# Kernel optimization log

Hardware: AMD Instinct MI355X
Metric: run time of the kernel (lower is better)

The kernel has to match this reference:

```python
import jax, jax.numpy as jnp
import numpy as np

B, S, D = 8, 2048, 256


def setup_inputs() -> dict:
    key = jax.random.key(0)
    k1, k2, k3, k4, k5 = jax.random.split(key, 5)
    head = jax.random.normal(k1, (B, S, D), dtype=jnp.float32)
    dep = jax.random.normal(k2, (B, S, D), dtype=jnp.float32)
    edge_U = jax.random.normal(k3, (D, D), dtype=jnp.float32) / np.sqrt(D)
    edge_W = jax.random.normal(k4, (1, 2 * D), dtype=jnp.float32) / np.sqrt(2 * D)
    edge_b = jax.random.normal(k5, (1,), dtype=jnp.float32)
    return {"head": head, "dep": dep, "edge_U": edge_U, "edge_W": edge_W, "edge_b": edge_b}


def reference(head, dep, edge_U, edge_W, edge_b):
    # t1[b,i,o] = head[b,i,:] @ U @ dep[b,o,:]  -> [B,S,S]
    t1 = jnp.einsum('bid,de,boe->bio', head, edge_U, dep)
    # t2: linear over pairwise concat(head_i, dep_o); decomposes into two
    # broadcast-added matvecs (same math as W @ concat, no [B,S^2,2D] tensor).
    d = head.shape[-1]
    wh, wd = edge_W[0, :d], edge_W[0, d:]
    hs = head @ wh  # [B,S]
    ds = dep @ wd   # [B,S]
    t2 = hs[:, :, None] + ds[:, None, :]  # [B,S,S]
    return t1 + t2 + edge_b[0]
```

## Files before the change

kernel.cpp:

```cpp
#include <hip/hip_runtime.h>
#include <hip/hip_bf16.h>
#include <stdint.h>
#include <stddef.h>

#define B_ 8
#define S_ 2048
#define D_ 256
#define NROWS (B_ * S_)

typedef __attribute__((ext_vector_type(8))) short short8;
typedef __attribute__((ext_vector_type(4))) short short4v;
typedef __attribute__((ext_vector_type(4))) float f32x4;

__device__ __forceinline__ short bf16of(float f) {
  union { float f; unsigned u; } x; x.f = f;
  unsigned r = x.u + 0x7FFFu + ((x.u >> 16) & 1u);
  return (short)(r >> 16);
}

__global__ void k_prep_u(const float* __restrict__ U, short* __restrict__ UT) {
  int n = blockIdx.x;
  int k = threadIdx.x;
  UT[n * D_ + k] = bf16of(U[k * D_ + n]);
}

__global__ void k_rows(const float* __restrict__ head, const float* __restrict__ dep,
                       const float* __restrict__ W,
                       float* __restrict__ hs, float* __restrict__ ds,
                       short* __restrict__ headB, short* __restrict__ depB) {
  const float* X; const float* wv; float* sv; short* XB;
  if (blockIdx.y == 0) { X = head; wv = W;      sv = hs; XB = headB; }
  else                 { X = dep;  wv = W + D_; sv = ds; XB = depB;  }
  const int row = blockIdx.x * 4 + (threadIdx.x >> 6);
  const int l = threadIdx.x & 63;
  const float4 v  = *(const float4*)(X + (size_t)row * D_ + l * 4);
  const float4 wq = *(const float4*)(wv + l * 4);
  short4v pk;
  pk[0] = bf16of(v.x); pk[1] = bf16of(v.y); pk[2] = bf16of(v.z); pk[3] = bf16of(v.w);
  *(short4v*)(XB + (size_t)row * D_ + l * 4) = pk;
  float p = v.x * wq.x + v.y * wq.y + v.z * wq.z + v.w * wq.w;
  p += __shfl_xor(p, 1); p += __shfl_xor(p, 2); p += __shfl_xor(p, 4);
  p += __shfl_xor(p, 8); p += __shfl_xor(p, 16); p += __shfl_xor(p, 32);
  if (l == 0) sv[row] = p;
}

__launch_bounds__(256, 3)
__global__ void k_ahat(const short* __restrict__ headB, const short* __restrict__ UT,
                       short* __restrict__ Ahat) {
  const int t = threadIdx.x;
  const int w = t >> 6;
  const int l = t & 63;
  const int quad = l >> 4;
  const int r15 = l & 15;
  const int nbase = blockIdx.x * 128;
  const int mbase = blockIdx.y * 128;

  const short* pA = UT + (size_t)(nbase + (w >> 1) * 64 + r15) * D_ + quad * 8;
  const short* pB = headB + (size_t)(mbase + (w & 1) * 64 + r15) * D_ + quad * 8;

  f32x4 acc[4][4];
#pragma unroll
  for (int i = 0; i < 4; ++i)
#pragma unroll
    for (int j = 0; j < 4; ++j) acc[i][j] = (f32x4)0.0f;

#pragma unroll 2
  for (int k0 = 0; k0 < D_; k0 += 32) {
    short8 aF[4], bF[4];
#pragma unroll
    for (int mt = 0; mt < 4; ++mt)
      aF[mt] = *(const short8*)(pA + (size_t)(mt * 16) * D_ + k0);
#pragma unroll
    for (int nt = 0; nt < 4; ++nt)
      bF[nt] = *(const short8*)(pB + (size_t)(nt * 16) * D_ + k0);
#pragma unroll
    for (int mt = 0; mt < 4; ++mt)
#pragma unroll
      for (int nt = 0; nt < 4; ++nt)
        acc[mt][nt] = __builtin_amdgcn_mfma_f32_16x16x32_bf16(aF[mt], bF[nt], acc[mt][nt], 0, 0, 0);
  }

#pragma unroll
  for (int mt = 0; mt < 4; ++mt) {
    int n_loc = (w >> 1) * 64 + mt * 16 + quad * 4;
#pragma unroll
    for (int nt = 0; nt < 4; ++nt) {
      int i_loc = (w & 1) * 64 + nt * 16 + r15;
      short4v pk;
      pk[0] = bf16of(acc[mt][nt][0]); pk[1] = bf16of(acc[mt][nt][1]);
      pk[2] = bf16of(acc[mt][nt][2]); pk[3] = bf16of(acc[mt][nt][3]);
      *(short4v*)(Ahat + (size_t)(mbase + i_loc) * D_ + nbase + n_loc) = pk;
    }
  }
}

__launch_bounds__(256, 3)
__global__ void k_main(const short* __restrict__ Ahat, const short* __restrict__ depB,
                       const float* __restrict__ hs, const float* __restrict__ ds,
                       const float* __restrict__ eb, float* __restrict__ out) {
  const int t = threadIdx.x;
  const int w = t >> 6;
  const int l = t & 63;
  const int quad = l >> 4;
  const int r15 = l & 15;
  const int b = blockIdx.z;
  const int mbase = blockIdx.y * 128;
  const int nbase = blockIdx.x * 128;

  const short* pA = depB + (size_t)(b * S_ + nbase + (w >> 1) * 64 + r15) * D_ + quad * 8;
  const short* pB = Ahat + (size_t)(b * S_ + mbase + (w & 1) * 64 + r15) * D_ + quad * 8;

  f32x4 acc[4][4];
#pragma unroll
  for (int i = 0; i < 4; ++i)
#pragma unroll
    for (int j = 0; j < 4; ++j) acc[i][j] = (f32x4)0.0f;

#pragma unroll 2
  for (int k0 = 0; k0 < D_; k0 += 32) {
    short8 aF[4], bF[4];
#pragma unroll
    for (int mt = 0; mt < 4; ++mt)
      aF[mt] = *(const short8*)(pA + (size_t)(mt * 16) * D_ + k0);
#pragma unroll
    for (int nt = 0; nt < 4; ++nt)
      bF[nt] = *(const short8*)(pB + (size_t)(nt * 16) * D_ + k0);
#pragma unroll
    for (int mt = 0; mt < 4; ++mt)
#pragma unroll
      for (int nt = 0; nt < 4; ++nt)
        acc[mt][nt] = __builtin_amdgcn_mfma_f32_16x16x32_bf16(aF[mt], bF[nt], acc[mt][nt], 0, 0, 0);
  }

  const float bias = eb[0];
  float hv4[4];
#pragma unroll
  for (int nt = 0; nt < 4; ++nt)
    hv4[nt] = hs[(size_t)b * S_ + mbase + (w & 1) * 64 + nt * 16 + r15] + bias;

#pragma unroll
  for (int mt = 0; mt < 4; ++mt) {
    int o_loc = (w >> 1) * 64 + mt * 16 + quad * 4;
    float4 dsv = *(const float4*)(ds + (size_t)b * S_ + nbase + o_loc);
#pragma unroll
    for (int nt = 0; nt < 4; ++nt) {
      int i_loc = (w & 1) * 64 + nt * 16 + r15;
      float hv = hv4[nt];
      f32x4 a = acc[mt][nt];
      float4 o4;
      o4.x = a[0] + hv + dsv.x;
      o4.y = a[1] + hv + dsv.y;
      o4.z = a[2] + hv + dsv.z;
      o4.w = a[3] + hv + dsv.w;
      *(float4*)(out + (size_t)(b * S_ + mbase + i_loc) * S_ + nbase + o_loc) = o4;
    }
  }
}

extern "C" void kernel_launch(void* const* d_in, const int* in_sizes, int n_in,
                              void* d_out, int out_size, void* d_ws, size_t ws_size,
                              hipStream_t stream) {
  const float* head = (const float*)d_in[0];
  const float* dep  = (const float*)d_in[1];
  const float* U    = (const float*)d_in[2];
  const float* W    = (const float*)d_in[3];
  const float* eb   = (const float*)d_in[4];
  float* out = (float*)d_out;

  char* ws = (char*)d_ws;
  short* UT    = (short*)ws;
  float* hs    = (float*)(ws + (128 << 10));
  float* ds    = (float*)(ws + (192 << 10));
  short* headB = (short*)(ws + (256 << 10));
  short* depB  = (short*)(ws + (256 << 10) + (8 << 20));
  short* Ahat  = (short*)(ws + (256 << 10) + (16 << 20));

  k_prep_u<<<dim3(256), dim3(256), 0, stream>>>(U, UT);
  k_rows<<<dim3(NROWS / 4, 2), dim3(256), 0, stream>>>(head, dep, W, hs, ds, headB, depB);
  k_ahat<<<dim3(2, 128), dim3(256), 0, stream>>>(headB, UT, Ahat);
  k_main<<<dim3(16, 16, 8), dim3(256), 0, stream>>>(Ahat, depB, hs, ds, eb, out);
}
```

Measured before the change: 236.9 us.

## Stage GEMM operand tiles through double-buffered LDS with async global loads

Both MFMA GEMM kernels now stage A and B tiles into XOR-swizzled shared memory using global_load_lds async copies. The copies are double-buffered over K chunks of 64, so loads for later chunks overlap with MFMA work on the current chunk. This replaces the per-lane direct global fragment loads, which were redundant across waves, with cooperative staging. In exchange it uses 64KB of LDS per block, lowers launch bounds occupancy from 3 to 2, and adds barriers and hand-written vmcnt waits.

```diff
diff --git a/kernel.cpp b/kernel.cpp
--- a/kernel.cpp
+++ b/kernel.cpp
@@ -16,6 +16,23 @@
   union { float f; unsigned u; } x; x.f = f;
   unsigned r = x.u + 0x7FFFu + ((x.u >> 16) & 1u);
   return (short)(r >> 16);
+}
+
+__device__ __forceinline__ void async_ld16(const void* g, void* s) {
+  __builtin_amdgcn_global_load_lds(
+      (const __attribute__((address_space(1))) void*)g,
+      (__attribute__((address_space(3))) void*)s, 16, 0, 0);
+}
+
+__device__ __forceinline__ void stage_tile(const short* __restrict__ g_row0,
+                                           char* lds_base, int t, int kk0) {
+#pragma unroll
+  for (int c = 0; c < 4; ++c) {
+    int p = c * 256 + t;
+    int r = p >> 3;
+    int sl = (p & 7) ^ (r & 7);
+    async_ld16(g_row0 + (size_t)r * D_ + kk0 + sl * 8, lds_base + p * 16);
+  }
 }
 
 __global__ void k_prep_u(const float* __restrict__ U, short* __restrict__ UT) {
@@ -44,19 +61,22 @@
   if (l == 0) sv[row] = p;
 }
 
-__launch_bounds__(256, 3)
+__launch_bounds__(256, 2)
 __global__ void k_ahat(const short* __restrict__ headB, const short* __restrict__ UT,
                        short* __restrict__ Ahat) {
+  __shared__ __align__(16) short sU[2 * 128 * 64];
+  __shared__ __align__(16) short sH[2 * 128 * 64];
   const int t = threadIdx.x;
   const int w = t >> 6;
   const int l = t & 63;
   const int quad = l >> 4;
   const int r15 = l & 15;
+  const int sw = r15 & 7;
   const int nbase = blockIdx.x * 128;
   const int mbase = blockIdx.y * 128;
 
-  const short* pA = UT + (size_t)(nbase + (w >> 1) * 64 + r15) * D_ + quad * 8;
-  const short* pB = headB + (size_t)(mbase + (w & 1) * 64 + r15) * D_ + quad * 8;
+  const short* gA = UT + (size_t)nbase * D_;
+  const short* gB = headB + (size_t)mbase * D_;
 
   f32x4 acc[4][4];
 #pragma unroll
@@ -64,20 +84,41 @@
 #pragma unroll
     for (int j = 0; j < 4; ++j) acc[i][j] = (f32x4)0.0f;
 
-#pragma unroll 2
-  for (int k0 = 0; k0 < D_; k0 += 32) {
-    short8 aF[4], bF[4];
-#pragma unroll
-    for (int mt = 0; mt < 4; ++mt)
-      aF[mt] = *(const short8*)(pA + (size_t)(mt * 16) * D_ + k0);
-#pragma unroll
-    for (int nt = 0; nt < 4; ++nt)
-      bF[nt] = *(const short8*)(pB + (size_t)(nt * 16) * D_ + k0);
-#pragma unroll
-    for (int mt = 0; mt < 4; ++mt)
-#pragma unroll
-      for (int nt = 0; nt < 4; ++nt)
-        acc[mt][nt] = __builtin_amdgcn_mfma_f32_16x16x32_bf16(aF[mt], bF[nt], acc[mt][nt], 0, 0, 0);
+  stage_tile(gA, (char*)sU, t, 0);
+  stage_tile(gB, (char*)sH, t, 0);
+  stage_tile(gA, (char*)sU + 16384, t, 64);
+  stage_tile(gB, (char*)sH + 16384, t, 64);
+
+  const int baseA = ((w >> 1) * 64 + r15) * 8;
+  const int baseB = ((w & 1) * 64 + r15) * 8;
+
+#pragma unroll
+  for (int it = 0; it < 4; ++it) {
+    if (it < 3) asm volatile("s_waitcnt vmcnt(8)" ::: "memory");
+    else        asm volatile("s_waitcnt vmcnt(0)" ::: "memory");
+    __builtin_amdgcn_s_barrier();
+
+    const short8* pA = (const short8*)(sU + (size_t)(it & 1) * (128 * 64));
+    const short8* pB = (const short8*)(sH + (size_t)(it & 1) * (128 * 64));
+#pragma unroll
+    for (int kb = 0; kb < 2; ++kb) {
+      const int so = (kb * 4 + quad) ^ sw;
+      short8 aF[4], bF[4];
+#pragma unroll
+      for (int mt = 0; mt < 4; ++mt) aF[mt] = pA[baseA + mt * 128 + so];
+#pragma unroll
+      for (int nt = 0; nt < 4; ++nt) bF[nt] = pB[baseB + nt * 128 + so];
+#pragma unroll
+      for (int mt = 0; mt < 4; ++mt)
+#pragma unroll
+        for (int nt = 0; nt < 4; ++nt)
+          acc[mt][nt] = __builtin_amdgcn_mfma_f32_16x16x32_bf16(aF[mt], bF[nt], acc[mt][nt], 0, 0, 0);
+    }
+    __builtin_amdgcn_s_barrier();
+    if (it < 2) {
+      stage_tile(gA, (char*)sU + (size_t)(it & 1) * 16384, t, (it + 2) * 64);
+      stage_tile(gB, (char*)sH + (size_t)(it & 1) * 16384, t, (it + 2) * 64);
+    }
   }
 
 #pragma unroll
@@ -94,21 +135,24 @@
   }
 }
 
-__launch_bounds__(256, 3)
+__launch_bounds__(256, 2)
 __global__ void k_main(const short* __restrict__ Ahat, const short* __restrict__ depB,
                        const float* __restrict__ hs, const float* __restrict__ ds,
                        const float* __restrict__ eb, float* __restrict__ out) {
+  __shared__ __align__(16) short sD[2 * 128 * 64];
+  __shared__ __align__(16) short sAh[2 * 128 * 64];
   const int t = threadIdx.x;
   const int w = t >> 6;
   const int l = t & 63;
   const int quad = l >> 4;
   const int r15 = l & 15;
+  const int sw = r15 & 7;
   const int b = blockIdx.z;
   const int mbase = blockIdx.y * 128;
   const int nbase = blockIdx.x * 128;
 
-  const short* pA = depB + (size_t)(b * S_ + nbase + (w >> 1) * 64 + r15) * D_ + quad * 8;
-  const short* pB = Ahat + (size_t)(b * S_ + mbase + (w & 1) * 64 + r15) * D_ + quad * 8;
+  const short* gA = depB + (size_t)(b * S_ + nbase) * D_;
+  const short* gB = Ahat + (size_t)(b * S_ + mbase) * D_;
 
   f32x4 acc[4][4];
 #pragma unroll
@@ -116,20 +160,41 @@
 #pragma unroll
     for (int j = 0; j < 4; ++j) acc[i][j] = (f32x4)0.0f;
 
-#pragma unroll 2
-  for (int k0 = 0; k0 < D_; k0 += 32) {
-    short8 aF[4], bF[4];
-#pragma unroll
-    for (int mt = 0; mt < 4; ++mt)
-      aF[mt] = *(const short8*)(pA + (size_t)(mt * 16) * D_ + k0);
-#pragma unroll
-    for (int nt = 0; nt < 4; ++nt)
-      bF[nt] = *(const short8*)(pB + (size_t)(nt * 16) * D_ + k0);
-#pragma unroll
-    for (int mt = 0; mt < 4; ++mt)
-#pragma unroll
-      for (int nt = 0; nt < 4; ++nt)
-        acc[mt][nt] = __builtin_amdgcn_mfma_f32_16x16x32_bf16(aF[mt], bF[nt], acc[mt][nt], 0, 0, 0);
+  stage_tile(gA, (char*)sD, t, 0);
+  stage_tile(gB, (char*)sAh, t, 0);
+  stage_tile(gA, (char*)sD + 16384, t, 64);
+  stage_tile(gB, (char*)sAh + 16384, t, 64);
+
+  const int baseA = ((w >> 1) * 64 + r15) * 8;
+  const int baseB = ((w & 1) * 64 + r15) * 8;
+
+#pragma unroll
+  for (int it = 0; it < 4; ++it) {
+    if (it < 3) asm volatile("s_waitcnt vmcnt(8)" ::: "memory");
+    else        asm volatile("s_waitcnt vmcnt(0)" ::: "memory");
+    __builtin_amdgcn_s_barrier();
+
+    const short8* pA = (const short8*)(sD + (size_t)(it & 1) * (128 * 64));
+    const short8* pB = (const short8*)(sAh + (size_t)(it & 1) * (128 * 64));
+#pragma unroll
+    for (int kb = 0; kb < 2; ++kb) {
+      const int so = (kb * 4 + quad) ^ sw;
+      short8 aF[4], bF[4];
+#pragma unroll
+      for (int mt = 0; mt < 4; ++mt) aF[mt] = pA[baseA + mt * 128 + so];
+#pragma unroll
+      for (int nt = 0; nt < 4; ++nt) bF[nt] = pB[baseB + nt * 128 + so];
+#pragma unroll
+      for (int mt = 0; mt < 4; ++mt)
+#pragma unroll
+        for (int nt = 0; nt < 4; ++nt)
+          acc[mt][nt] = __builtin_amdgcn_mfma_f32_16x16x32_bf16(aF[mt], bF[nt], acc[mt][nt], 0, 0, 0);
+    }
+    __builtin_amdgcn_s_barrier();
+    if (it < 2) {
+      stage_tile(gA, (char*)sD + (size_t)(it & 1) * 16384, t, (it + 2) * 64);
+      stage_tile(gB, (char*)sAh + (size_t)(it & 1) * 16384, t, (it + 2) * 64);
+    }
   }
 
   const float bias = eb[0];
```

Measured after the change: 194.0 us. -18.1%, faster.

## Fuse Ahat projection into main GEMM with async LDS-staged dep tiles

Applied to the files above, without the earlier changes.

Merges the head@U projection and the main bilinear GEMM into one kernel. Each block computes a 64-row Ahat tile into swizzled LDS, then streams 1024 dep rows through double-buffered LDS using global_load_lds async copies, writing outputs every 128 columns. This removes the Ahat global round trip and one kernel launch. In exchange each block recomputes its Ahat tile (twice per row block across the two column halves), runs with fewer blocks per CU, and relies on hand-placed waitcnt and barrier synchronization.

```diff
diff --git a/kernel.cpp b/kernel.cpp
--- a/kernel.cpp
+++ b/kernel.cpp
@@ -16,6 +16,23 @@
   union { float f; unsigned u; } x; x.f = f;
   unsigned r = x.u + 0x7FFFu + ((x.u >> 16) & 1u);
   return (short)(r >> 16);
+}
+
+__device__ __forceinline__ void async_ld16(const void* g, void* s) {
+  __builtin_amdgcn_global_load_lds(
+      (const __attribute__((address_space(1))) void*)g,
+      (__attribute__((address_space(3))) void*)s, 16, 0, 0);
+}
+
+__device__ __forceinline__ void stage_tile64(const short* __restrict__ g_row0,
+                                             char* lds_base, int t, int kk0) {
+#pragma unroll
+  for (int c = 0; c < 4; ++c) {
+    int p = c * 256 + t;
+    int r = p >> 3;
+    int sl = (p & 7) ^ (r & 7);
+    async_ld16(g_row0 + (size_t)r * D_ + kk0 + sl * 8, lds_base + p * 16);
+  }
 }
 
 __global__ void k_prep_u(const float* __restrict__ U, short* __restrict__ UT) {
@@ -44,115 +61,137 @@
   if (l == 0) sv[row] = p;
 }
 
-__launch_bounds__(256, 3)
-__global__ void k_ahat(const short* __restrict__ headB, const short* __restrict__ UT,
-                       short* __restrict__ Ahat) {
+__launch_bounds__(256, 2)
+__global__ void k_fused(const short* __restrict__ headB, const short* __restrict__ UT,
+                        const short* __restrict__ depB,
+                        const float* __restrict__ hs, const float* __restrict__ ds,
+                        const float* __restrict__ eb, float* __restrict__ out) {
+  __shared__ __align__(16) short sAh[64 * 256];
+  __shared__ __align__(16) short sD[2 * 128 * 64];
   const int t = threadIdx.x;
   const int w = t >> 6;
   const int l = t & 63;
   const int quad = l >> 4;
   const int r15 = l & 15;
-  const int nbase = blockIdx.x * 128;
-  const int mbase = blockIdx.y * 128;
-
-  const short* pA = UT + (size_t)(nbase + (w >> 1) * 64 + r15) * D_ + quad * 8;
-  const short* pB = headB + (size_t)(mbase + (w & 1) * 64 + r15) * D_ + quad * 8;
-
-  f32x4 acc[4][4];
-#pragma unroll
-  for (int i = 0; i < 4; ++i)
+  const int sw = r15 & 7;
+  const int oh = blockIdx.x;
+  const int ib = blockIdx.y;
+  const int b  = blockIdx.z;
+  const int irow0 = b * S_ + ib * 64;
+  const int orow0 = b * S_ + oh * 1024;
+  const int ocol0 = oh * 1024;
+
+  stage_tile64(depB + (size_t)orow0 * D_, (char*)sD, t, 0);
+  stage_tile64(depB + (size_t)orow0 * D_, (char*)sD + 16384, t, 64);
+
+  {
+    f32x4 accA[4][4];
+#pragma unroll
+    for (int i = 0; i < 4; ++i)
+#pragma unroll
+      for (int j = 0; j < 4; ++j) accA[i][j] = (f32x4)0.0f;
+
+    const short* pUg = UT + (size_t)(w * 64 + r15) * D_ + quad * 8;
+    const short* pHg = headB + (size_t)(irow0 + r15) * D_ + quad * 8;
+#pragma unroll 2
+    for (int k0 = 0; k0 < D_; k0 += 32) {
+      short8 aF[4], bF[4];
+#pragma unroll
+      for (int ar = 0; ar < 4; ++ar)
+        aF[ar] = *(const short8*)(pUg + (size_t)(ar * 16) * D_ + k0);
+#pragma unroll
+      for (int nt = 0; nt < 4; ++nt)
+        bF[nt] = *(const short8*)(pHg + (size_t)(nt * 16) * D_ + k0);
+#pragma unroll
+      for (int ar = 0; ar < 4; ++ar)
+#pragma unroll
+        for (int nt = 0; nt < 4; ++nt)
+          accA[ar][nt] = __builtin_amdgcn_mfma_f32_16x16x32_bf16(aF[ar], bF[nt], accA[ar][nt], 0, 0, 0);
+    }
+
+#pragma unroll
+    for (int ar = 0; ar < 4; ++ar) {
+      const int ncol = w * 64 + ar * 16 + quad * 4;
+      const int slot = ncol >> 3;
+      const int half = (ncol >> 2) & 1;
+#pragma unroll
+      for (int nt = 0; nt < 4; ++nt) {
+        const int i = nt * 16 + r15;
+        const int sp = (slot & 24) | ((slot ^ i) & 7);
+        short4v pk;
+        pk[0] = bf16of(accA[ar][nt][0]); pk[1] = bf16of(accA[ar][nt][1]);
+        pk[2] = bf16of(accA[ar][nt][2]); pk[3] = bf16of(accA[ar][nt][3]);
+        *(short4v*)((char*)sAh + (size_t)i * 512 + sp * 16 + half * 8) = pk;
+      }
+    }
+  }
+  asm volatile("s_waitcnt lgkmcnt(0)" ::: "memory");
+  __builtin_amdgcn_s_barrier();
+
+  f32x4 acc[2][4];
+#pragma unroll
+  for (int i = 0; i < 2; ++i)
 #pragma unroll
     for (int j = 0; j < 4; ++j) acc[i][j] = (f32x4)0.0f;
 
-#pragma unroll 2
-  for (int k0 = 0; k0 < D_; k0 += 32) {
-    short8 aF[4], bF[4];
-#pragma unroll
-    for (int mt = 0; mt < 4; ++mt)
-      aF[mt] = *(const short8*)(pA + (size_t)(mt * 16) * D_ + k0);
-#pragma unroll
-    for (int nt = 0; nt < 4; ++nt)
-      bF[nt] = *(const short8*)(pB + (size_t)(nt * 16) * D_ + k0);
-#pragma unroll
-    for (int mt = 0; mt < 4; ++mt)
+  const float bias = eb[0];
+  float hv[4];
+#pragma unroll
+  for (int nt = 0; nt < 4; ++nt)
+    hv[nt] = hs[irow0 + nt * 16 + r15] + bias;
+
+  for (int s = 0; s < 32; ++s) {
+    if (s < 31) asm volatile("s_waitcnt vmcnt(4)" ::: "memory");
+    else        asm volatile("s_waitcnt vmcnt(0)" ::: "memory");
+    __builtin_amdgcn_s_barrier();
+
+    const short8* pA = (const short8*)(sD + (size_t)(s & 1) * (128 * 64));
+    const short8* pB = (const short8*)sAh;
+#pragma unroll
+    for (int ks = 0; ks < 2; ++ks) {
+      const int soA = (ks * 4 + quad) ^ sw;
+      const int sgB = (s & 3) * 8 + ks * 4 + quad;
+      const int soB = (sgB & 24) | ((sgB ^ r15) & 7);
+      short8 aF[2], bF[4];
+#pragma unroll
+      for (int mt = 0; mt < 2; ++mt)
+        aF[mt] = pA[(w * 32 + mt * 16 + r15) * 8 + soA];
 #pragma unroll
       for (int nt = 0; nt < 4; ++nt)
-        acc[mt][nt] = __builtin_amdgcn_mfma_f32_16x16x32_bf16(aF[mt], bF[nt], acc[mt][nt], 0, 0, 0);
-  }
-
-#pragma unroll
-  for (int mt = 0; mt < 4; ++mt) {
-    int n_loc = (w >> 1) * 64 + mt * 16 + quad * 4;
-#pragma unroll
-    for (int nt = 0; nt < 4; ++nt) {
-      int i_loc = (w & 1) * 64 + nt * 16 + r15;
-      short4v pk;
-      pk[0] = bf16of(acc[mt][nt][0]); pk[1] = bf16of(acc[mt][nt][1]);
-      pk[2] = bf16of(acc[mt][nt][2]); pk[3] = bf16of(acc[mt][nt][3]);
-      *(short4v*)(Ahat + (size_t)(mbase + i_loc) * D_ + nbase + n_loc) = pk;
-    }
-  }
-}
-
-__launch_bounds__(256, 3)
-__global__ void k_main(const short* __restrict__ Ahat, const short* __restrict__ depB,
-                       const float* __restrict__ hs, const float* __restrict__ ds,
-                       const float* __restrict__ eb, float* __restrict__ out) {
-  const int t = threadIdx.x;
-  const int w = t >> 6;
-  const int l = t & 63;
-  const int quad = l >> 4;
-  const int r15 = l & 15;
-  const int b = blockIdx.z;
-  const int mbase = blockIdx.y * 128;
-  const int nbase = blockIdx.x * 128;
-
-  const short* pA = depB + (size_t)(b * S_ + nbase + (w >> 1) * 64 + r15) * D_ + quad * 8;
-  const short* pB = Ahat + (size_t)(b * S_ + mbase + (w & 1) * 64 + r15) * D_ + quad * 8;
-
-  f32x4 acc[4][4];
-#pragma unroll
-  for (int i = 0; i < 4; ++i)
-#pragma unroll
-    for (int j = 0; j < 4; ++j) acc[i][j] = (f32x4)0.0f;
-
-#pragma unroll 2
-  for (int k0 = 0; k0 < D_; k0 += 32) {
-    short8 aF[4], bF[4];
-#pragma unroll
-    for (int mt = 0; mt < 4; ++mt)
-      aF[mt] = *(const short8*)(pA + (size_t)(mt * 16) * D_ + k0);
-#pragma unroll
-    for (int nt = 0; nt < 4; ++nt)
-      bF[nt] = *(const short8*)(pB + (size_t)(nt * 16) * D_ + k0);
-#pragma unroll
-    for (int mt = 0; mt < 4; ++mt)
-#pragma unroll
-      for (int nt = 0; nt < 4; ++nt)
-        acc[mt][nt] = __builtin_amdgcn_mfma_f32_16x16x32_bf16(aF[mt], bF[nt], acc[mt][nt], 0, 0, 0);
-  }
-
-  const float bias = eb[0];
-  float hv4[4];
-#pragma unroll
-  for (int nt = 0; nt < 4; ++nt)
-    hv4[nt] = hs[(size_t)b * S_ + mbase + (w & 1) * 64 + nt * 16 + r15] + bias;
-
-#pragma unroll
-  for (int mt = 0; mt < 4; ++mt) {
-    int o_loc = (w >> 1) * 64 + mt * 16 + quad * 4;
-    float4 dsv = *(const float4*)(ds + (size_t)b * S_ + nbase + o_loc);
-#pragma unroll
-    for (int nt = 0; nt < 4; ++nt) {
-      int i_loc = (w & 1) * 64 + nt * 16 + r15;
-      float hv = hv4[nt];
-      f32x4 a = acc[mt][nt];
-      float4 o4;
-      o4.x = a[0] + hv + dsv.x;
-      o4.y = a[1] + hv + dsv.y;
-      o4.z = a[2] + hv + dsv.z;
-      o4.w = a[3] + hv + dsv.w;
-      *(float4*)(out + (size_t)(b * S_ + mbase + i_loc) * S_ + nbase + o_loc) = o4;
+        bF[nt] = pB[(nt * 16 + r15) * 32 + soB];
+#pragma unroll
+      for (int mt = 0; mt < 2; ++mt)
+#pragma unroll
+        for (int nt = 0; nt < 4; ++nt)
+          acc[mt][nt] = __builtin_amdgcn_mfma_f32_16x16x32_bf16(aF[mt], bF[nt], acc[mt][nt], 0, 0, 0);
+    }
+    __builtin_amdgcn_s_barrier();
+
+    if (s < 30) {
+      const int s2 = s + 2;
+      stage_tile64(depB + (size_t)(orow0 + (s2 >> 2) * 128) * D_,
+                   (char*)sD + (size_t)(s & 1) * 16384, t, (s2 & 3) * 64);
+    }
+
+    if ((s & 3) == 3) {
+      const int ot = s >> 2;
+#pragma unroll
+      for (int mt = 0; mt < 2; ++mt) {
+        const int o_loc = w * 32 + mt * 16 + quad * 4;
+        f32x4 dsv = *(const f32x4*)(ds + orow0 + ot * 128 + o_loc);
+#pragma unroll
+        for (int nt = 0; nt < 4; ++nt) {
+          const int i = nt * 16 + r15;
+          f32x4 a = acc[mt][nt];
+          f32x4 o4;
+          o4[0] = a[0] + hv[nt] + dsv[0];
+          o4[1] = a[1] + hv[nt] + dsv[1];
+          o4[2] = a[2] + hv[nt] + dsv[2];
+          o4[3] = a[3] + hv[nt] + dsv[3];
+          *(f32x4*)(out + (size_t)(irow0 + i) * S_ + ocol0 + ot * 128 + o_loc) = o4;
+          acc[mt][nt] = (f32x4)0.0f;
+        }
+      }
     }
   }
 }
@@ -173,10 +212,8 @@
   float* ds    = (float*)(ws + (192 << 10));
   short* headB = (short*)(ws + (256 << 10));
   short* depB  = (short*)(ws + (256 << 10) + (8 << 20));
-  short* Ahat  = (short*)(ws + (256 << 10) + (16 << 20));
 
   k_prep_u<<<dim3(256), dim3(256), 0, stream>>>(U, UT);
   k_rows<<<dim3(NROWS / 4, 2), dim3(256), 0, stream>>>(head, dep, W, hs, ds, headB, depB);
-  k_ahat<<<dim3(2, 128), dim3(256), 0, stream>>>(headB, UT, Ahat);
-  k_main<<<dim3(16, 16, 8), dim3(256), 0, stream>>>(Ahat, depB, hs, ds, eb, out);
-}
+  k_fused<<<dim3(2, 32, 8), dim3(256), 0, stream>>>(headB, UT, depB, hs, ds, eb, out);
+}
```

Result: faster. 198.1 us (-16.4%).
